# Performance work log

Measured on AMD Instinct MI355X. Metric: run time of the kernel, lower is better.

The kernel has to match this reference:

```python
import jax, jax.numpy as jnp
import numpy as np

N, K, D = 131072, 2048, 512


def setup_inputs() -> dict:
    key = jax.random.key(0)
    kx, kc = jax.random.split(key)
    x = jax.random.normal(kx, (N, D), dtype=jnp.float32)
    cluster_centers = jax.random.normal(kc, (K, D), dtype=jnp.float32)
    return {"x": x, "cluster_centers": cluster_centers}


def reference(x, cluster_centers):
    # d_{nk} = ||x_n - c_k||_2; argmin over k.
    x2 = jnp.sum(x * x, axis=-1, keepdims=True)            # [N,1]
    c2 = jnp.sum(cluster_centers * cluster_centers, -1)    # [K]
    d2 = x2 + c2 - 2.0 * (x @ cluster_centers.T)           # [N,K]
    # sqrt is monotonic, so argmin over squared distances equals argmin over L2 norms
    return jnp.argmin(d2, axis=-1)                          # [N] int
```

## Files before the change

### kernel.cpp

```cpp
#include <hip/hip_runtime.h>


#define N_PTS 131072
#define K_CL  2048
#define D_DIM 512
#define BM 128
#define BN 128
#define BK 32
#define NKT (K_CL / BN)
#define NDT (D_DIM / BK)
#define NT  (NKT * NDT)

typedef _Float16 half8  __attribute__((ext_vector_type(8)));
typedef _Float16 half4v __attribute__((ext_vector_type(4)));
typedef float    floatx4 __attribute__((ext_vector_type(4)));

#define GLL(g, l) __builtin_amdgcn_global_load_lds( \
    (__attribute__((address_space(1))) void*)(g),   \
    (__attribute__((address_space(3))) void*)(l), 16, 0, 0)

__global__ void row_norms_kernel(const float* __restrict__ A,
                                 float* __restrict__ out, int rows) {
    int gid  = blockIdx.x * blockDim.x + threadIdx.x;
    int wave = gid >> 6;
    int lane = gid & 63;
    if (wave >= rows) return;
    const float4* a = (const float4*)(A + (size_t)wave * D_DIM);
    float4 p = a[lane];
    float4 q = a[lane + 64];
    float s = p.x*p.x + p.y*p.y + p.z*p.z + p.w*p.w
            + q.x*q.x + q.y*q.y + q.z*q.z + q.w*q.w;
    #pragma unroll
    for (int off = 32; off > 0; off >>= 1) s += __shfl_down(s, off, 64);
    if (lane == 0) out[wave] = s;
}

__global__ void conv_f16x2_kernel(const float* __restrict__ src,
                                  _Float16* __restrict__ hi,
                                  _Float16* __restrict__ lo, int n4) {
    int i = blockIdx.x * blockDim.x + threadIdx.x;
    if (i >= n4) return;
    float4 v = ((const float4*)src)[i];
    half4v h, l;
    h.x = (_Float16)v.x; h.y = (_Float16)v.y;
    h.z = (_Float16)v.z; h.w = (_Float16)v.w;
    l.x = (_Float16)(v.x - (float)h.x);
    l.y = (_Float16)(v.y - (float)h.y);
    l.z = (_Float16)(v.z - (float)h.z);
    l.w = (_Float16)(v.w - (float)h.w);
    *(half4v*)(hi + (size_t)i * 4) = h;
    *(half4v*)(lo + (size_t)i * 4) = l;
}

template<bool XPRE, bool CPRE>
__global__ __launch_bounds__(256, 2)
void kmeans_mfma(const float* __restrict__ X, const float* __restrict__ C,
                 const _Float16* __restrict__ Xhi, const _Float16* __restrict__ Xlo,
                 const _Float16* __restrict__ Chi, const _Float16* __restrict__ Clo,
                 const float* __restrict__ c2g, int* __restrict__ out) {
    __shared__ __align__(16) _Float16 sXh[2][BM * BK], sXl[2][BM * BK];
    __shared__ __align__(16) _Float16 sCh[2][BN * BK], sCl[2][BN * BK];
    __shared__ float c2s[K_CL];
    __shared__ float x2s[BM];

    const int tid  = threadIdx.x;
    const int lane = tid & 63;
    const int w    = tid >> 6;
    const int wti  = w >> 1;
    const int wtj  = w & 1;
    const int q    = lane >> 4;
    const int m16  = lane & 15;
    const int rowBase = blockIdx.x * BM;

    const int jsrc = (((lane & 3) ^ ((lane >> 3) & 3)) * 8);
    const int swq8 = ((q ^ ((m16 >> 1) & 3)) * 8);

    if (CPRE) {
        for (int i = tid; i < K_CL / 4; i += 256)
            ((float4*)c2s)[i] = ((const float4*)c2g)[i];
    } else {
        for (int k = tid; k < K_CL; k += 256) {
            const float4* cp = (const float4*)(C + (size_t)k * D_DIM);
            float s0 = 0.f, s1 = 0.f;
            for (int j = 0; j < D_DIM / 4; j += 2) {
                float4 a = cp[j], b = cp[j + 1];
                s0 += a.x*a.x + a.y*a.y + a.z*a.z + a.w*a.w;
                s1 += b.x*b.x + b.y*b.y + b.z*b.z + b.w*b.w;
            }
            c2s[k] = s0 + s1;
        }
    }
    {
        int r = tid & 127, h = tid >> 7;
        const float4* xp = (const float4*)(X + (size_t)(rowBase + r) * D_DIM + h * 256);
        float s0 = 0.f, s1 = 0.f;
        for (int j = 0; j < 64; j += 2) {
            float4 a = xp[j], b = xp[j + 1];
            s0 += a.x*a.x + a.y*a.y + a.z*a.z + a.w*a.w;
            s1 += b.x*b.x + b.y*b.y + b.z*b.z + b.w*b.w;
        }
        ((float*)sXh)[tid] = s0 + s1;
    }
    __syncthreads();
    if (tid < BM) x2s[tid] = ((float*)sXh)[tid] + ((float*)sXh)[tid + 128];
    __syncthreads();

    const int s_c4 = tid & 7;
    const int s_r0 = tid >> 3;

    auto stage = [&](int t) {
        const int dtl = t & (NDT - 1);
        const int ktl = t >> 4;
        const int d0  = dtl * BK;
        const int k0l = ktl * BN;
        const int b   = t & 1;
        _Float16* dXh = sXh[b]; _Float16* dXl = sXl[b];
        _Float16* dCh = sCh[b]; _Float16* dCl = sCl[b];
        if constexpr (XPRE) {
            #pragma unroll
            for (int s = 0; s < 2; ++s) {
                const int cc = w * 2 + s;
                const int r  = cc * 16 + (lane >> 2);
                const size_t go = (size_t)(rowBase + r) * D_DIM + d0 + jsrc;
                GLL(Xhi + go, &dXh[cc * 512]);
                GLL(Xlo + go, &dXl[cc * 512]);
            }
        } else {
            #pragma unroll
            for (int p = 0; p < 4; ++p) {
                const int r = s_r0 + p * 32;
                float4 v = *(const float4*)&X[(size_t)(rowBase + r) * D_DIM + d0 + s_c4 * 4];
                half4v h, l;
                h.x = (_Float16)v.x; h.y = (_Float16)v.y;
                h.z = (_Float16)v.z; h.w = (_Float16)v.w;
                l.x = (_Float16)(v.x - (float)h.x);
                l.y = (_Float16)(v.y - (float)h.y);
                l.z = (_Float16)(v.z - (float)h.z);
                l.w = (_Float16)(v.w - (float)h.w);
                const int off = r * BK + (((s_c4 >> 1) ^ ((r >> 1) & 3)) * 8) + (s_c4 & 1) * 4;
                *(half4v*)&dXh[off] = h;
                *(half4v*)&dXl[off] = l;
            }
        }
        if constexpr (CPRE) {
            #pragma unroll
            for (int s = 0; s < 2; ++s) {
                const int cc = w * 2 + s;
                const int r  = cc * 16 + (lane >> 2);
                const size_t go = (size_t)(k0l + r) * D_DIM + d0 + jsrc;
                GLL(Chi + go, &dCh[cc * 512]);
                GLL(Clo + go, &dCl[cc * 512]);
            }
        } else {
            #pragma unroll
            for (int p = 0; p < 4; ++p) {
                const int r = s_r0 + p * 32;
                float4 v = *(const float4*)&C[(size_t)(k0l + r) * D_DIM + d0 + s_c4 * 4];
                half4v h, l;
                h.x = (_Float16)v.x; h.y = (_Float16)v.y;
                h.z = (_Float16)v.z; h.w = (_Float16)v.w;
                l.x = (_Float16)(v.x - (float)h.x);
                l.y = (_Float16)(v.y - (float)h.y);
                l.z = (_Float16)(v.z - (float)h.z);
                l.w = (_Float16)(v.w - (float)h.w);
                const int off = r * BK + (((s_c4 >> 1) ^ ((r >> 1) & 3)) * 8) + (s_c4 & 1) * 4;
                *(half4v*)&dCh[off] = h;
                *(half4v*)&dCl[off] = l;
            }
        }
    };

    float bestV[4][4];
    int   bestI[4][4];
    #pragma unroll
    for (int ti = 0; ti < 4; ++ti)
        #pragma unroll
        for (int r = 0; r < 4; ++r) { bestV[ti][r] = 3.4e38f; bestI[ti][r] = 0; }

    stage(0);
    __syncthreads();

    #pragma unroll 1
    for (int kt = 0; kt < NKT; ++kt) {
        const int k0 = kt * BN;
        floatx4 acc[4][4];
        #pragma unroll
        for (int ti = 0; ti < 4; ++ti)
            #pragma unroll
            for (int tj = 0; tj < 4; ++tj) acc[ti][tj] = (floatx4){0.f, 0.f, 0.f, 0.f};

        #pragma unroll 2
        for (int dt = 0; dt < NDT; ++dt) {
            const int t = kt * NDT + dt;
            if (t + 1 < NT) stage(t + 1);

            const int b = t & 1;
            const _Float16* bXh = sXh[b]; const _Float16* bXl = sXl[b];
            const _Float16* bCh = sCh[b]; const _Float16* bCl = sCl[b];

            half8 ah[4], al[4];
            #pragma unroll
            for (int ti = 0; ti < 4; ++ti) {
                const int row = wti * 64 + ti * 16 + m16;
                ah[ti] = *(const half8*)&bXh[row * BK + swq8];
                al[ti] = *(const half8*)&bXl[row * BK + swq8];
            }
            __builtin_amdgcn_s_setprio(1);
            #pragma unroll
            for (int tj = 0; tj < 4; ++tj) {
                const int col = wtj * 64 + tj * 16 + m16;
                half8 bh = *(const half8*)&bCh[col * BK + swq8];
                half8 bl = *(const half8*)&bCl[col * BK + swq8];
                #pragma unroll
                for (int ti = 0; ti < 4; ++ti) {
                    floatx4 a = acc[ti][tj];
                    a = __builtin_amdgcn_mfma_f32_16x16x32_f16(ah[ti], bh, a, 0, 0, 0);
                    a = __builtin_amdgcn_mfma_f32_16x16x32_f16(ah[ti], bl, a, 0, 0, 0);
                    a = __builtin_amdgcn_mfma_f32_16x16x32_f16(al[ti], bh, a, 0, 0, 0);
                    acc[ti][tj] = a;
                }
            }
            __builtin_amdgcn_s_setprio(0);
            __syncthreads();
        }

        #pragma unroll
        for (int tj = 0; tj < 4; ++tj) {
            int col = k0 + wtj * 64 + tj * 16 + m16;
            float cv = c2s[col];
            #pragma unroll
            for (int ti = 0; ti < 4; ++ti)
                #pragma unroll
                for (int r = 0; r < 4; ++r) {
                    float s = x2s[wti * 64 + ti * 16 + q * 4 + r] + cv;
                    float v = s - 2.0f * acc[ti][tj][r];
                    if (v < bestV[ti][r]) { bestV[ti][r] = v; bestI[ti][r] = col; }
                }
        }
    }

    #pragma unroll
    for (int ti = 0; ti < 4; ++ti)
        #pragma unroll
        for (int r = 0; r < 4; ++r) {
            float v = bestV[ti][r]; int ix = bestI[ti][r];
            #pragma unroll
            for (int off = 1; off < 16; off <<= 1) {
                float ov = __shfl_xor(v, off, 64);
                int   oi = __shfl_xor(ix, off, 64);
                if (ov < v || (ov == v && oi < ix)) { v = ov; ix = oi; }
            }
            bestV[ti][r] = v; bestI[ti][r] = ix;
        }

    __syncthreads();
    float* rv  = (float*)sXh;
    int*   rix = (int*)sCh;
    if (m16 == 0) {
        #pragma unroll
        for (int ti = 0; ti < 4; ++ti)
            #pragma unroll
            for (int r = 0; r < 4; ++r) {
                int rloc = wti * 64 + ti * 16 + q * 4 + r;
                rv[rloc * 2 + wtj]  = bestV[ti][r];
                rix[rloc * 2 + wtj] = bestI[ti][r];
            }
    }
    __syncthreads();
    if (tid < BM) {
        float v0 = rv[tid * 2], v1 = rv[tid * 2 + 1];
        int   i0 = rix[tid * 2], i1 = rix[tid * 2 + 1];
        out[rowBase + tid] = (v1 < v0 || (v1 == v0 && i1 < i0)) ? i1 : i0;
    }
}

extern "C" void kernel_launch(void* const* d_in, const int* in_sizes, int n_in,
                              void* d_out, int out_size, void* d_ws, size_t ws_size,
                              hipStream_t stream) {
    const float* X = (const float*)d_in[0];
    const float* C = (const float*)d_in[1];
    int* out = (int*)d_out;

    char* ws = (char*)d_ws;
    const size_t c2_off  = 0;
    const size_t chi_off = (size_t)K_CL * 4;
    const size_t clo_off = chi_off + (size_t)K_CL * D_DIM * 2;
    const size_t xhi_off = clo_off + (size_t)K_CL * D_DIM * 2;
    const size_t xlo_off = xhi_off + (size_t)N_PTS * D_DIM * 2;
    const size_t need_C    = xhi_off;
    const size_t need_full = xlo_off + (size_t)N_PTS * D_DIM * 2;

    if (ws_size >= need_full) {
        float*    c2  = (float*)(ws + c2_off);
        _Float16* Chi = (_Float16*)(ws + chi_off);
        _Float16* Clo = (_Float16*)(ws + clo_off);
        _Float16* Xhi = (_Float16*)(ws + xhi_off);
        _Float16* Xlo = (_Float16*)(ws + xlo_off);
        row_norms_kernel<<<(K_CL * 64) / 256, 256, 0, stream>>>(C, c2, K_CL);
        conv_f16x2_kernel<<<(K_CL * D_DIM / 4) / 256, 256, 0, stream>>>(
            C, Chi, Clo, K_CL * D_DIM / 4);
        conv_f16x2_kernel<<<(N_PTS * D_DIM / 4 + 255) / 256, 256, 0, stream>>>(
            X, Xhi, Xlo, N_PTS * D_DIM / 4);
        kmeans_mfma<true, true><<<N_PTS / BM, 256, 0, stream>>>(
            X, C, Xhi, Xlo, Chi, Clo, c2, out);
    } else if (ws_size >= need_C) {
        float*    c2  = (float*)(ws + c2_off);
        _Float16* Chi = (_Float16*)(ws + chi_off);
        _Float16* Clo = (_Float16*)(ws + clo_off);
        row_norms_kernel<<<(K_CL * 64) / 256, 256, 0, stream>>>(C, c2, K_CL);
        conv_f16x2_kernel<<<(K_CL * D_DIM / 4) / 256, 256, 0, stream>>>(
            C, Chi, Clo, K_CL * D_DIM / 4);
        kmeans_mfma<false, true><<<N_PTS / BM, 256, 0, stream>>>(
            X, C, nullptr, nullptr, Chi, Clo, c2, out);
    } else {
        kmeans_mfma<false, false><<<N_PTS / BM, 256, 0, stream>>>(
            X, C, nullptr, nullptr, nullptr, nullptr, nullptr, out);
    }
}
```

Baseline: 1.277 ms.

## Prefetch two tiles ahead with explicit vmcnt waits instead of full syncthreads

Restructures the double-buffered K-loop so all LDS fragments are read into registers first, then a barrier frees the buffer and the tile two steps ahead is issued via global_load_lds before the MFMA block. When both operands are pre-split, full __syncthreads are replaced with s_waitcnt vmcnt(8)/lgkmcnt(0) plus raw s_barrier, so in-flight async loads need not drain each iteration. This aims to hide global load latency behind more compute, at the cost of extra registers for B fragments and reliance on a hand-tuned vmcnt count matching the number of loads per stage.

Result: faster. 1.215 ms (-4.9%).

```diff
diff --git a/kernel.cpp b/kernel.cpp
--- a/kernel.cpp
+++ b/kernel.cpp
@@ -58,6 +58,8 @@
                  const _Float16* __restrict__ Xhi, const _Float16* __restrict__ Xlo,
                  const _Float16* __restrict__ Chi, const _Float16* __restrict__ Clo,
                  const float* __restrict__ c2g, int* __restrict__ out) {
+    constexpr bool ASYNC = XPRE && CPRE;
+
     __shared__ __align__(16) _Float16 sXh[2][BM * BK], sXl[2][BM * BK];
     __shared__ __align__(16) _Float16 sCh[2][BN * BK], sCl[2][BN * BK];
     __shared__ float c2s[K_CL];
@@ -178,7 +180,13 @@
         for (int r = 0; r < 4; ++r) { bestV[ti][r] = 3.4e38f; bestI[ti][r] = 0; }
 
     stage(0);
-    __syncthreads();
+    stage(1);
+    if constexpr (ASYNC) {
+        asm volatile("s_waitcnt vmcnt(8)" ::: "memory");
+        __builtin_amdgcn_s_barrier();
+    } else {
+        __syncthreads();
+    }
 
     #pragma unroll 1
     for (int kt = 0; kt < NKT; ++kt) {
@@ -192,36 +200,55 @@
         #pragma unroll 2
         for (int dt = 0; dt < NDT; ++dt) {
             const int t = kt * NDT + dt;
-            if (t + 1 < NT) stage(t + 1);
-
             const int b = t & 1;
             const _Float16* bXh = sXh[b]; const _Float16* bXl = sXl[b];
             const _Float16* bCh = sCh[b]; const _Float16* bCl = sCl[b];
 
-            half8 ah[4], al[4];
+            half8 ah[4], al[4], bh[4], bl[4];
             #pragma unroll
             for (int ti = 0; ti < 4; ++ti) {
                 const int row = wti * 64 + ti * 16 + m16;
                 ah[ti] = *(const half8*)&bXh[row * BK + swq8];
                 al[ti] = *(const half8*)&bXl[row * BK + swq8];
             }
-            __builtin_amdgcn_s_setprio(1);
             #pragma unroll
             for (int tj = 0; tj < 4; ++tj) {
                 const int col = wtj * 64 + tj * 16 + m16;
-                half8 bh = *(const half8*)&bCh[col * BK + swq8];
-                half8 bl = *(const half8*)&bCl[col * BK + swq8];
+                bh[tj] = *(const half8*)&bCh[col * BK + swq8];
+                bl[tj] = *(const half8*)&bCl[col * BK + swq8];
+            }
+
+            if constexpr (ASYNC) {
+                asm volatile("s_waitcnt lgkmcnt(0)" ::: "memory");
+                __builtin_amdgcn_sched_barrier(0);
+                __builtin_amdgcn_s_barrier();
+            } else {
+                __syncthreads();
+            }
+
+            if (t + 2 < NT) stage(t + 2);
+
+            __builtin_amdgcn_s_setprio(1);
+            #pragma unroll
+            for (int tj = 0; tj < 4; ++tj) {
                 #pragma unroll
                 for (int ti = 0; ti < 4; ++ti) {
                     floatx4 a = acc[ti][tj];
-                    a = __builtin_amdgcn_mfma_f32_16x16x32_f16(ah[ti], bh, a, 0, 0, 0);
-                    a = __builtin_amdgcn_mfma_f32_16x16x32_f16(ah[ti], bl, a, 0, 0, 0);
-                    a = __builtin_amdgcn_mfma_f32_16x16x32_f16(al[ti], bh, a, 0, 0, 0);
+                    a = __builtin_amdgcn_mfma_f32_16x16x32_f16(ah[ti], bh[tj], a, 0, 0, 0);
+                    a = __builtin_amdgcn_mfma_f32_16x16x32_f16(ah[ti], bl[tj], a, 0, 0, 0);
+                    a = __builtin_amdgcn_mfma_f32_16x16x32_f16(al[ti], bh[tj], a, 0, 0, 0);
                     acc[ti][tj] = a;
                 }
             }
             __builtin_amdgcn_s_setprio(0);
-            __syncthreads();
+
+            if constexpr (ASYNC) {
+                if (t + 2 < NT) asm volatile("s_waitcnt vmcnt(8)" ::: "memory");
+                else            asm volatile("s_waitcnt vmcnt(0)" ::: "memory");
+                __builtin_amdgcn_s_barrier();
+            } else {
+                __syncthreads();
+            }
         }
 
         #pragma unroll
```

## Enlarge row tile to 256 and add triple-buffered async LDS pipeline

Applied to the files above, without the earlier changes.

Doubles the block row tile to 256 with 512 threads, so each C tile loaded into LDS is reused by more rows. Staging becomes a three-deep ring of LDS buffers filled by global_load_lds. It uses manual vmcnt/lgkmcnt waits and raw barriers instead of __syncthreads, and double-buffers the MFMA fragments in registers so the next tile's LDS reads overlap the current MFMAs. The cost is much higher LDS use (about 150KB per block), which limits the CU to one block, plus hand-tuned wait counts that are fragile and wait more conservatively than the pipeline depth needs.

Result: slower. 1.358 ms (+6.4%).

```diff
diff --git a/kernel.cpp b/kernel.cpp
--- a/kernel.cpp
+++ b/kernel.cpp
@@ -4,12 +4,15 @@
 #define N_PTS 131072
 #define K_CL  2048
 #define D_DIM 512
-#define BM 128
+#define BM 256
 #define BN 128
 #define BK 32
+#define THREADS 512
 #define NKT (K_CL / BN)
 #define NDT (D_DIM / BK)
 #define NT  (NKT * NDT)
+#define XPLANE (BM * BK)
+#define CPLANE (BN * BK)
 
 typedef _Float16 half8  __attribute__((ext_vector_type(8)));
 typedef _Float16 half4v __attribute__((ext_vector_type(4)));
@@ -53,13 +56,15 @@
 }
 
 template<bool XPRE, bool CPRE>
-__global__ __launch_bounds__(256, 2)
+__global__ __launch_bounds__(THREADS, 2)
 void kmeans_mfma(const float* __restrict__ X, const float* __restrict__ C,
                  const _Float16* __restrict__ Xhi, const _Float16* __restrict__ Xlo,
                  const _Float16* __restrict__ Chi, const _Float16* __restrict__ Clo,
                  const float* __restrict__ c2g, int* __restrict__ out) {
-    __shared__ __align__(16) _Float16 sXh[2][BM * BK], sXl[2][BM * BK];
-    __shared__ __align__(16) _Float16 sCh[2][BN * BK], sCl[2][BN * BK];
+    constexpr bool ASYNC = XPRE && CPRE;
+
+    __shared__ __align__(16) _Float16 sXh[3][XPLANE], sXl[3][XPLANE];
+    __shared__ __align__(16) _Float16 sCh[3][CPLANE], sCl[3][CPLANE];
     __shared__ float c2s[K_CL];
     __shared__ float x2s[BM];
 
@@ -76,10 +81,10 @@
     const int swq8 = ((q ^ ((m16 >> 1) & 3)) * 8);
 
     if (CPRE) {
-        for (int i = tid; i < K_CL / 4; i += 256)
+        for (int i = tid; i < K_CL / 4; i += THREADS)
             ((float4*)c2s)[i] = ((const float4*)c2g)[i];
     } else {
-        for (int k = tid; k < K_CL; k += 256) {
+        for (int k = tid; k < K_CL; k += THREADS) {
             const float4* cp = (const float4*)(C + (size_t)k * D_DIM);
             float s0 = 0.f, s1 = 0.f;
             for (int j = 0; j < D_DIM / 4; j += 2) {
@@ -91,7 +96,7 @@
         }
     }
     {
-        int r = tid & 127, h = tid >> 7;
+        int r = tid & (BM - 1), h = tid >> 8;
         const float4* xp = (const float4*)(X + (size_t)(rowBase + r) * D_DIM + h * 256);
         float s0 = 0.f, s1 = 0.f;
         for (int j = 0; j < 64; j += 2) {
@@ -102,18 +107,17 @@
         ((float*)sXh)[tid] = s0 + s1;
     }
     __syncthreads();
-    if (tid < BM) x2s[tid] = ((float*)sXh)[tid] + ((float*)sXh)[tid + 128];
+    if (tid < BM) x2s[tid] = ((float*)sXh)[tid] + ((float*)sXh)[tid + BM];
     __syncthreads();
 
     const int s_c4 = tid & 7;
     const int s_r0 = tid >> 3;
 
-    auto stage = [&](int t) {
+    auto stage = [&](int t, int b) {
         const int dtl = t & (NDT - 1);
         const int ktl = t >> 4;
         const int d0  = dtl * BK;
         const int k0l = ktl * BN;
-        const int b   = t & 1;
         _Float16* dXh = sXh[b]; _Float16* dXl = sXl[b];
         _Float16* dCh = sCh[b]; _Float16* dCl = sCl[b];
         if constexpr (XPRE) {
@@ -128,7 +132,7 @@
         } else {
             #pragma unroll
             for (int p = 0; p < 4; ++p) {
-                const int r = s_r0 + p * 32;
+                const int r = s_r0 + p * 64;
                 float4 v = *(const float4*)&X[(size_t)(rowBase + r) * D_DIM + d0 + s_c4 * 4];
                 half4v h, l;
                 h.x = (_Float16)v.x; h.y = (_Float16)v.y;
@@ -143,18 +147,14 @@
             }
         }
         if constexpr (CPRE) {
-            #pragma unroll
-            for (int s = 0; s < 2; ++s) {
-                const int cc = w * 2 + s;
-                const int r  = cc * 16 + (lane >> 2);
-                const size_t go = (size_t)(k0l + r) * D_DIM + d0 + jsrc;
-                GLL(Chi + go, &dCh[cc * 512]);
-                GLL(Clo + go, &dCl[cc * 512]);
-            }
+            const int r = w * 16 + (lane >> 2);
+            const size_t go = (size_t)(k0l + r) * D_DIM + d0 + jsrc;
+            GLL(Chi + go, &dCh[w * 512]);
+            GLL(Clo + go, &dCl[w * 512]);
         } else {
             #pragma unroll
-            for (int p = 0; p < 4; ++p) {
-                const int r = s_r0 + p * 32;
+            for (int p = 0; p < 2; ++p) {
+                const int r = s_r0 + p * 64;
                 float4 v = *(const float4*)&C[(size_t)(k0l + r) * D_DIM + d0 + s_c4 * 4];
                 half4v h, l;
                 h.x = (_Float16)v.x; h.y = (_Float16)v.y;
@@ -170,6 +170,53 @@
         }
     };
 
+    half8 fah[2][4], fal[2][4], fbh[2][4], fbl[2][4];
+    floatx4 acc[4][4];
+
+    #define READ_FRAGS(B_, S_) do {                                        \
+        const _Float16* xh_ = sXh[B_]; const _Float16* xl_ = sXl[B_];      \
+        const _Float16* ch_ = sCh[B_]; const _Float16* cl_ = sCl[B_];      \
+        _Pragma("unroll")                                                  \
+        for (int ti_ = 0; ti_ < 4; ++ti_) {                                \
+            const int row_ = wti * 64 + ti_ * 16 + m16;                    \
+            fah[S_][ti_] = *(const half8*)&xh_[row_ * BK + swq8];          \
+            fal[S_][ti_] = *(const half8*)&xl_[row_ * BK + swq8];          \
+        }                                                                  \
+        _Pragma("unroll")                                                  \
+        for (int tj_ = 0; tj_ < 4; ++tj_) {                                \
+            const int col_ = wtj * 64 + tj_ * 16 + m16;                    \
+            fbh[S_][tj_] = *(const half8*)&ch_[col_ * BK + swq8];          \
+            fbl[S_][tj_] = *(const half8*)&cl_[col_ * BK + swq8];          \
+        }                                                                  \
+    } while (0)
+
+    #define MFMA48(S_) do {                                                \
+        __builtin_amdgcn_s_setprio(1);                                     \
+        _Pragma("unroll")                                                  \
+        for (int tj_ = 0; tj_ < 4; ++tj_)                                  \
+            _Pragma("unroll")                                              \
+            for (int ti_ = 0; ti_ < 4; ++ti_) {                            \
+                floatx4 a_ = acc[ti_][tj_];                                \
+                a_ = __builtin_amdgcn_mfma_f32_16x16x32_f16(fah[S_][ti_], fbh[S_][tj_], a_, 0, 0, 0); \
+                a_ = __builtin_amdgcn_mfma_f32_16x16x32_f16(fah[S_][ti_], fbl[S_][tj_], a_, 0, 0, 0); \
+                a_ = __builtin_amdgcn_mfma_f32_16x16x32_f16(fal[S_][ti_], fbh[S_][tj_], a_, 0, 0, 0); \
+                acc[ti_][tj_] = a_;                                        \
+            }                                                              \
+        __builtin_amdgcn_s_setprio(0);                                     \
+    } while (0)
+
+    #define ITER(T_, CUR_, NXT_) do {                                       \
+        if ((T_) + 3 < NT) stage((T_) + 3, bS);                             \
+        if ((T_) + 1 < NT) READ_FRAGS(bR, NXT_);                            \
+        MFMA48(CUR_);                                                       \
+        asm volatile("s_waitcnt lgkmcnt(0)" ::: "memory");                  \
+        if ((T_) + 3 < NT) asm volatile("s_waitcnt vmcnt(6)" ::: "memory"); \
+        else               asm volatile("s_waitcnt vmcnt(0)" ::: "memory"); \
+        __builtin_amdgcn_s_barrier();                                       \
+        bR = (bR == 2) ? 0 : bR + 1;                                        \
+        bS = (bS == 2) ? 0 : bS + 1;                                        \
+    } while (0)
+
     float bestV[4][4];
     int   bestI[4][4];
     #pragma unroll
@@ -177,51 +224,41 @@
         #pragma unroll
         for (int r = 0; r < 4; ++r) { bestV[ti][r] = 3.4e38f; bestI[ti][r] = 0; }
 
-    stage(0);
-    __syncthreads();
+    int bR = 1, bS = 0;
+    if constexpr (ASYNC) {
+        stage(0, 0); stage(1, 1); stage(2, 2);
+        asm volatile("s_waitcnt vmcnt(6)" ::: "memory");
+        __builtin_amdgcn_s_barrier();
+        READ_FRAGS(0, 0);
+        asm volatile("s_waitcnt lgkmcnt(0)" ::: "memory");
+        __builtin_amdgcn_s_barrier();
+    }
 
     #pragma unroll 1
     for (int kt = 0; kt < NKT; ++kt) {
         const int k0 = kt * BN;
-        floatx4 acc[4][4];
         #pragma unroll
         for (int ti = 0; ti < 4; ++ti)
             #pragma unroll
             for (int tj = 0; tj < 4; ++tj) acc[ti][tj] = (floatx4){0.f, 0.f, 0.f, 0.f};
 
-        #pragma unroll 2
-        for (int dt = 0; dt < NDT; ++dt) {
-            const int t = kt * NDT + dt;
-            if (t + 1 < NT) stage(t + 1);
-
-            const int b = t & 1;
-            const _Float16* bXh = sXh[b]; const _Float16* bXl = sXl[b];
-            const _Float16* bCh = sCh[b]; const _Float16* bCl = sCl[b];
-
-            half8 ah[4], al[4];
-            #pragma unroll
-            for (int ti = 0; ti < 4; ++ti) {
-                const int row = wti * 64 + ti * 16 + m16;
-                ah[ti] = *(const half8*)&bXh[row * BK + swq8];
-                al[ti] = *(const half8*)&bXl[row * BK + swq8];
-            }
-            __builtin_amdgcn_s_setprio(1);
-            #pragma unroll
-            for (int tj = 0; tj < 4; ++tj) {
-                const int col = wtj * 64 + tj * 16 + m16;
-                half8 bh = *(const half8*)&bCh[col * BK + swq8];
-                half8 bl = *(const half8*)&bCl[col * BK + swq8];
-                #pragma unroll
-                for (int ti = 0; ti < 4; ++ti) {
-                    floatx4 a = acc[ti][tj];
-                    a = __builtin_amdgcn_mfma_f32_16x16x32_f16(ah[ti], bh, a, 0, 0, 0);
-                    a = __builtin_amdgcn_mfma_f32_16x16x32_f16(ah[ti], bl, a, 0, 0, 0);
-                    a = __builtin_amdgcn_mfma_f32_16x16x32_f16(al[ti], bh, a, 0, 0, 0);
-                    acc[ti][tj] = a;
-                }
-            }
-            __builtin_amdgcn_s_setprio(0);
-            __syncthreads();
+        if constexpr (ASYNC) {
+            #pragma unroll 1
+            for (int dt = 0; dt < NDT; dt += 2) {
+                const int t = kt * NDT + dt;
+                ITER(t,     0, 1);
+                ITER(t + 1, 1, 0);
+            }
+        } else {
+            #pragma unroll 1
+            for (int dt = 0; dt < NDT; ++dt) {
+                const int t = kt * NDT + dt;
+                __syncthreads();
+                stage(t, 0);
+                __syncthreads();
+                READ_FRAGS(0, 0);
+                MFMA48(0);
+            }
         }
 
         #pragma unroll
@@ -238,6 +275,9 @@
                 }
         }
     }
+    #undef ITER
+    #undef MFMA48
+    #undef READ_FRAGS
 
     #pragma unroll
     for (int ti = 0; ti < 4; ++ti)
@@ -301,7 +341,7 @@
             C, Chi, Clo, K_CL * D_DIM / 4);
         conv_f16x2_kernel<<<(N_PTS * D_DIM / 4 + 255) / 256, 256, 0, stream>>>(
             X, Xhi, Xlo, N_PTS * D_DIM / 4);
-        kmeans_mfma<true, true><<<N_PTS / BM, 256, 0, stream>>>(
+        kmeans_mfma<true, true><<<N_PTS / BM, THREADS, 0, stream>>>(
             X, C, Xhi, Xlo, Chi, Clo, c2, out);
     } else if (ws_size >= need_C) {
         float*    c2  = (float*)(ws + c2_off);
@@ -310,10 +350,10 @@
         row_norms_kernel<<<(K_CL * 64) / 256, 256, 0, stream>>>(C, c2, K_CL);
         conv_f16x2_kernel<<<(K_CL * D_DIM / 4) / 256, 256, 0, stream>>>(
             C, Chi, Clo, K_CL * D_DIM / 4);
-        kmeans_mfma<false, true><<<N_PTS / BM, 256, 0, stream>>>(
+        kmeans_mfma<false, true><<<N_PTS / BM, THREADS, 0, stream>>>(
             X, C, nullptr, nullptr, Chi, Clo, c2, out);
     } else {
-        kmeans_mfma<false, false><<<N_PTS / BM, 256, 0, stream>>>(
+        kmeans_mfma<false, false><<<N_PTS / BM, THREADS, 0, stream>>>(
             X, C, nullptr, nullptr, nullptr, nullptr, nullptr, out);
     }
 }
```
